# Kernel optimization log

Hardware: AMD Instinct MI355X
Metric: run time of the kernel (lower is better)

The kernel has to match this reference:

```python
import jax, jax.numpy as jnp
import numpy as np

D_MODEL = 1024
N_HEADS = 16
HEAD_DIM = D_MODEL // N_HEADS
MAX_LEN = 2048
BATCH = 2
SEQ = 2048


def setup_inputs() -> dict:
    key = jax.random.key(0)
    ks = jax.random.split(key, 6)
    std = 1.0 / np.sqrt(D_MODEL)
    x = jax.random.normal(ks[0], (BATCH, SEQ, D_MODEL), dtype=jnp.float32)
    Wqkv = jax.random.uniform(ks[1], (D_MODEL, 3 * D_MODEL), minval=-std, maxval=std, dtype=jnp.float32)
    bqkv = jax.random.uniform(ks[2], (3 * D_MODEL,), minval=-std, maxval=std, dtype=jnp.float32)
    Wout = jax.random.uniform(ks[3], (D_MODEL, D_MODEL), minval=-std, maxval=std, dtype=jnp.float32)
    bout = jax.random.uniform(ks[4], (D_MODEL,), minval=-std, maxval=std, dtype=jnp.float32)
    rel_pos_bias = 0.02 * jax.random.normal(ks[5], (2 * MAX_LEN - 1,), dtype=jnp.float32)
    return {"x": x, "Wqkv": Wqkv, "bqkv": bqkv, "Wout": Wout, "bout": bout, "rel_pos_bias": rel_pos_bias}


def reference(x, Wqkv, bqkv, Wout, bout, rel_pos_bias):
    B, S, _ = x.shape
    scale = HEAD_DIM ** -0.5
    qkv = x @ Wqkv + bqkv                       # [B,S,3*dm]
    qkv = qkv.reshape(B, S, 3, N_HEADS, HEAD_DIM)
    qkv = jnp.transpose(qkv, (2, 0, 3, 1, 4))   # [3,B,H,S,D]
    q, k, v = qkv[0], qkv[1], qkv[2]
    scores = jnp.einsum('bhqd,bhkd->bhqk', q, k) * scale
    pos = jnp.arange(S)
    rel = jnp.clip(pos[:, None] - pos[None, :] + (MAX_LEN - 1), 0, 2 * MAX_LEN - 2)
    scores = scores + rel_pos_bias[rel][None, None]  # bias shared over batch & heads
    probs = jax.nn.softmax(scores, axis=-1)
    out = jnp.einsum('bhqk,bhkd->bhqd', probs, v)    # [B,H,S,D]
    out = jnp.transpose(out, (0, 2, 1, 3)).reshape(B, S, D_MODEL)
    return out @ Wout + bout
```

## Files before the change

kernel.cpp:

```cpp
#include <hip/hip_runtime.h>
#include <cmath>

#define B_ 2
#define S_ 2048
#define H_ 16
#define D_ 64
#define DM 1024

typedef unsigned short u16;
using short8 = __attribute__((ext_vector_type(8))) short;
using f32x4  = __attribute__((ext_vector_type(4))) float;
using f32x16 = __attribute__((ext_vector_type(16))) float;
using i32x4  = __attribute__((ext_vector_type(4))) int;
typedef float uf4 __attribute__((ext_vector_type(4), aligned(4)));

__device__ __forceinline__ u16 f32_to_bf16(float f) {
    unsigned int u = __float_as_uint(f);
    u += 0x7fffu + ((u >> 16) & 1u);
    return (u16)(u >> 16);
}

__device__ __forceinline__ float exp2_fast(float x) {
    float r;
    asm("v_exp_f32 %0, %1" : "=v"(r) : "v"(x));
    return r;
}

__device__ __forceinline__ int cvt_pk_bf16(float lo, float hi) {
    int r;
    asm("v_cvt_pk_bf16_f32 %0, %1, %2" : "=v"(r) : "v"(lo), "v"(hi));
    return r;
}

__device__ __forceinline__ void gl_lds16(const void* src, void* dst) {
    __builtin_amdgcn_global_load_lds(
        (const __attribute__((address_space(1))) unsigned int*)src,
        (__attribute__((address_space(3))) unsigned int*)dst, 16, 0, 0);
}

__device__ __forceinline__ f32x16 mfma32(short8 a, short8 b, f32x16 c) {
    return __builtin_amdgcn_mfma_f32_32x32x16_bf16(a, b, c, 0, 0, 0);
}

__global__ __launch_bounds__(256) void relattn_prep(
    const float* __restrict__ x, const float* __restrict__ Wqkv,
    const float* __restrict__ Wout, const float* __restrict__ relb,
    u16* __restrict__ xb, u16* __restrict__ WqkvT, u16* __restrict__ WoutT,
    float* __restrict__ relb2)
{
    __shared__ float T[64][65];
    const int tid = threadIdx.x;
    int blk = blockIdx.x;
    if (blk >= 3072) {
        int i0 = ((blk - 3072) * 256 + tid) * 4;
#pragma unroll
        for (int j = 0; j < 4; ++j)
            if (i0 + j < 2 * 2048 - 1)
                relb2[i0 + j] = relb[i0 + j] * 1.44269504f;
        return;
    }
    if (blk < 2048) {
        size_t base = ((size_t)blk * 256 + tid) * 8;
        float4 v0 = *(const float4*)(x + base);
        float4 v1 = *(const float4*)(x + base + 4);
        ushort4 p0 = make_ushort4(f32_to_bf16(v0.x), f32_to_bf16(v0.y),
                                  f32_to_bf16(v0.z), f32_to_bf16(v0.w));
        ushort4 p1 = make_ushort4(f32_to_bf16(v1.x), f32_to_bf16(v1.y),
                                  f32_to_bf16(v1.z), f32_to_bf16(v1.w));
        *(ushort4*)(xb + base) = p0;
        *(ushort4*)(xb + base + 4) = p1;
        return;
    }
    int id = blk - 2048;
    const float* in; u16* outp; int R, C;
    if (id < 768) { in = Wqkv; outp = WqkvT; R = 1024; C = 3072; }
    else          { id -= 768; in = Wout;  outp = WoutT; R = 1024; C = 1024; }
    const int tpr = C >> 6;
    const int r0 = (id / tpr) << 6, c0 = (id % tpr) << 6;
#pragma unroll
    for (int it = 0; it < 4; ++it) {
        int e = tid + it * 256;
        int row = e >> 4, c4 = (e & 15) << 2;
        float4 v = *(const float4*)(in + (size_t)(r0 + row) * C + c0 + c4);
        T[row][c4 + 0] = v.x; T[row][c4 + 1] = v.y;
        T[row][c4 + 2] = v.z; T[row][c4 + 3] = v.w;
    }
    __syncthreads();
#pragma unroll
    for (int it = 0; it < 4; ++it) {
        int e = tid + it * 256;
        int crow = e >> 4, r4 = (e & 15) << 2;
        ushort4 pk = make_ushort4(f32_to_bf16(T[r4 + 0][crow]), f32_to_bf16(T[r4 + 1][crow]),
                                  f32_to_bf16(T[r4 + 2][crow]), f32_to_bf16(T[r4 + 3][crow]));
        *(ushort4*)(outp + (size_t)(c0 + crow) * R + r0 + r4) = pk;
    }
}

__global__ __launch_bounds__(256) void relattn_gemm_qkv(
    const u16* __restrict__ A, const u16* __restrict__ Bm,
    const float* __restrict__ bias, u16* __restrict__ qk, u16* __restrict__ Vt)
{
    __shared__ alignas(16) unsigned char AsB[16384];
    __shared__ alignas(16) unsigned char BsB[16384];
    const int tid = threadIdx.x;
    const int w = tid >> 6, l = tid & 63, ln = l & 15, hi = l >> 4;
    const int wr = w >> 1, wc = w & 1;
    const int row0 = blockIdx.y * 128, col0 = blockIdx.x * 128;
    const char* Ab = (const char*)A;
    const char* Bb = (const char*)Bm;

    f32x4 acc[4][4] = {};
    for (int step = 0; step < 16; ++step) {
        __syncthreads();
#pragma unroll
        for (int it = 0; it < 4; ++it) {
            int dsto = it * 4096 + w * 1024;
            int o = dsto + l * 16;
            int row = o >> 7;
            int swz = (o & 127) ^ ((row & 7) << 4);
            gl_lds16(Ab + (size_t)(row0 + row) * 2048 + step * 128 + swz, AsB + dsto);
            gl_lds16(Bb + (size_t)(col0 + row) * 2048 + step * 128 + swz, BsB + dsto);
        }
        __syncthreads();
#pragma unroll
        for (int kk = 0; kk < 2; ++kk) {
            short8 a[4], b[4];
            const int kb = hi * 16 + kk * 64;
#pragma unroll
            for (int m = 0; m < 4; ++m) {
                int row = wr * 64 + m * 16 + ln;
                a[m] = *(const short8*)(AsB + row * 128 + (kb ^ ((row & 7) << 4)));
            }
#pragma unroll
            for (int n = 0; n < 4; ++n) {
                int row = wc * 64 + n * 16 + ln;
                b[n] = *(const short8*)(BsB + row * 128 + (kb ^ ((row & 7) << 4)));
            }
#pragma unroll
            for (int m = 0; m < 4; ++m)
#pragma unroll
                for (int n = 0; n < 4; ++n)
                    acc[m][n] = __builtin_amdgcn_mfma_f32_16x16x32_bf16(a[m], b[n], acc[m][n], 0, 0, 0);
        }
    }

    const int t = col0 >> 10;
    const int bb = row0 >> 11;
    if (t < 2) {
#pragma unroll
        for (int n = 0; n < 4; ++n) {
            int c = col0 + wc * 64 + n * 16 + ln;
            int h = (c >> 6) & 15, d = c & 63;
            float bv = bias[c];
            u16* plane = qk + (size_t)((t * B_ + bb) * H_ + h) * S_ * D_;
#pragma unroll
            for (int m = 0; m < 4; ++m)
#pragma unroll
                for (int r = 0; r < 4; ++r) {
                    int s = (row0 + wr * 64 + m * 16 + hi * 4 + r) & (S_ - 1);
                    plane[(size_t)s * D_ + d] = f32_to_bf16(acc[m][n][r] + bv);
                }
        }
    } else {
#pragma unroll
        for (int n = 0; n < 4; ++n) {
            int c = col0 + wc * 64 + n * 16 + ln;
            int h = (c >> 6) & 15, d = c & 63;
            float bv = bias[c];
            u16* vrow = Vt + (size_t)((bb * H_ + h) * D_ + d) * S_;
#pragma unroll
            for (int m = 0; m < 4; ++m) {
                int s = (row0 + wr * 64 + m * 16 + hi * 4) & (S_ - 1);
                ushort4 pk = make_ushort4(f32_to_bf16(acc[m][n][0] + bv),
                                          f32_to_bf16(acc[m][n][1] + bv),
                                          f32_to_bf16(acc[m][n][2] + bv),
                                          f32_to_bf16(acc[m][n][3] + bv));
                *(ushort4*)(vrow + s) = pk;
            }
        }
    }
}

__global__ __launch_bounds__(512, 4) void relattn_attn(
    const u16* __restrict__ qk, const u16* __restrict__ Vt,
    const float* __restrict__ relb2, u16* __restrict__ aout)
{
    __shared__ alignas(16) unsigned char Lds[65536];
    const int tid = threadIdx.x;
    const int w = tid >> 6, l = tid & 63;
    const int wg = w & 3, g = w >> 2;
    const int l31 = l & 31, h2 = l >> 5;
    const int qt = blockIdx.x, bh = blockIdx.y;
    const int bb = bh >> 4;
    const char* qpl = (const char*)(qk + (size_t)bh * (S_ * D_));
    const char* kpl = (const char*)(qk + (size_t)(B_ * H_ + bh) * (S_ * D_));
    const char* vpl = (const char*)(Vt + (size_t)bh * (D_ * S_));
    unsigned char* GB = Lds + g * 32768;

    const int q0 = qt * 128 + wg * 32;
    const int qrow = q0 + l31;
    const int kvbase = g * 1024;

    short8 qf[4];
#pragma unroll
    for (int kd = 0; kd < 4; ++kd)
        qf[kd] = *(const short8*)(qpl + (size_t)qrow * 128 + kd * 32 + h2 * 16);

    f32x16 O0 = {}, O1 = {};
    float mrun = -1e30f, lrun = 0.f;

    {
#pragma unroll
        for (int it = 0; it < 2; ++it) {
            int dsto = it * 4096 + wg * 1024;
            int o = dsto + l * 16;
            int row = o >> 7;
            int swz = (o & 127) ^ ((row & 7) << 4);
            gl_lds16(kpl + (size_t)(kvbase + row) * 128 + swz, GB + dsto);
            gl_lds16(vpl + (size_t)row * (S_ * 2) + kvbase * 2 + swz, GB + 8192 + dsto);
        }
    }
    __syncthreads();

    for (int kt = 0; kt < 16; ++kt) {
        const int buf = kt & 1;
        const unsigned char* KB = GB + buf * 16384;
        const unsigned char* VB = KB + 8192;
        const int kv0 = kvbase + kt * 64;

        if (kt < 15) {
#pragma unroll
            for (int it = 0; it < 2; ++it) {
                int dsto = it * 4096 + wg * 1024;
                int o = dsto + l * 16;
                int row = o >> 7;
                int swz = (o & 127) ^ ((row & 7) << 4);
                unsigned char* db = GB + (buf ^ 1) * 16384 + dsto;
                gl_lds16(kpl + (size_t)(kv0 + 64 + row) * 128 + swz, db);
                gl_lds16(vpl + (size_t)row * (S_ * 2) + (kv0 + 64) * 2 + swz, db + 8192);
            }
        }

        const float* bp0 = relb2 + (qrow - kv0 - 4 * h2 + 2047);
        uf4 bv0[4], bv1[4];
#pragma unroll
        for (int rq = 0; rq < 4; ++rq) {
            bv0[rq] = *(const uf4*)(bp0 - 8 * rq - 3);
            bv1[rq] = *(const uf4*)(bp0 - 32 - 8 * rq - 3);
        }

        f32x16 s0 = {}, s1 = {};
        __builtin_amdgcn_s_setprio(1);
#pragma unroll
        for (int kd = 0; kd < 4; ++kd) {
            int kbyte = kd * 32 + h2 * 16;
            int sw = (l31 & 7) << 4;
            short8 k0 = *(const short8*)(KB + l31 * 128 + (kbyte ^ sw));
            short8 k1 = *(const short8*)(KB + (32 + l31) * 128 + (kbyte ^ sw));
            s0 = mfma32(k0, qf[kd], s0);
            s1 = mfma32(k1, qf[kd], s1);
        }
        __builtin_amdgcn_s_setprio(0);

        const float SC2 = 0.125f * 1.44269504f;
#pragma unroll
        for (int rq = 0; rq < 4; ++rq)
#pragma unroll
            for (int j = 0; j < 4; ++j) {
                s0[rq * 4 + j] = s0[rq * 4 + j] * SC2 + bv0[rq][3 - j];
                s1[rq * 4 + j] = s1[rq * 4 + j] * SC2 + bv1[rq][3 - j];
            }

        float a0 = fmaxf(fmaxf(s0[0], s0[1]), fmaxf(s0[2], s0[3]));
        float a1 = fmaxf(fmaxf(s0[4], s0[5]), fmaxf(s0[6], s0[7]));
        float a2 = fmaxf(fmaxf(s0[8], s0[9]), fmaxf(s0[10], s0[11]));
        float a3 = fmaxf(fmaxf(s0[12], s0[13]), fmaxf(s0[14], s0[15]));
        float a4 = fmaxf(fmaxf(s1[0], s1[1]), fmaxf(s1[2], s1[3]));
        float a5 = fmaxf(fmaxf(s1[4], s1[5]), fmaxf(s1[6], s1[7]));
        float a6 = fmaxf(fmaxf(s1[8], s1[9]), fmaxf(s1[10], s1[11]));
        float a7 = fmaxf(fmaxf(s1[12], s1[13]), fmaxf(s1[14], s1[15]));
        float tm = fmaxf(fmaxf(fmaxf(a0, a1), fmaxf(a2, a3)),
                         fmaxf(fmaxf(a4, a5), fmaxf(a6, a7)));
        tm = fmaxf(tm, __shfl_xor(tm, 32));

        if (!__all(tm - mrun <= 8.0f)) {
            float nm = fmaxf(mrun, tm);
            float al = exp2_fast(mrun - nm);
            mrun = nm;
            lrun *= al;
#pragma unroll
            for (int r = 0; r < 16; ++r) { O0[r] *= al; O1[r] *= al; }
        }

#pragma unroll
        for (int r = 0; r < 16; ++r) s0[r] = exp2_fast(s0[r] - mrun);
#pragma unroll
        for (int r = 0; r < 16; ++r) s1[r] = exp2_fast(s1[r] - mrun);
        float q0s = ((s0[0] + s0[1]) + (s0[2] + s0[3])) + ((s0[4] + s0[5]) + (s0[6] + s0[7]));
        float q1s = ((s0[8] + s0[9]) + (s0[10] + s0[11])) + ((s0[12] + s0[13]) + (s0[14] + s0[15]));
        float q2s = ((s1[0] + s1[1]) + (s1[2] + s1[3])) + ((s1[4] + s1[5]) + (s1[6] + s1[7]));
        float q3s = ((s1[8] + s1[9]) + (s1[10] + s1[11])) + ((s1[12] + s1[13]) + (s1[14] + s1[15]));
        float ps = (q0s + q1s) + (q2s + q3s);
        ps += __shfl_xor(ps, 32);
        lrun += ps;

        __builtin_amdgcn_s_setprio(1);
#pragma unroll
        for (int ts = 0; ts < 4; ++ts) {
            float p0, p1, p2, p3, p4, p5, p6, p7;
            if (ts == 0)      { p0=s0[0];  p1=s0[1];  p2=s0[2];  p3=s0[3];  p4=s0[4];  p5=s0[5];  p6=s0[6];  p7=s0[7]; }
            else if (ts == 1) { p0=s0[8];  p1=s0[9];  p2=s0[10]; p3=s0[11]; p4=s0[12]; p5=s0[13]; p6=s0[14]; p7=s0[15]; }
            else if (ts == 2) { p0=s1[0];  p1=s1[1];  p2=s1[2];  p3=s1[3];  p4=s1[4];  p5=s1[5];  p6=s1[6];  p7=s1[7]; }
            else              { p0=s1[8];  p1=s1[9];  p2=s1[10]; p3=s1[11]; p4=s1[12]; p5=s1[13]; p6=s1[14]; p7=s1[15]; }
            int c01 = cvt_pk_bf16(p0, p1), c23 = cvt_pk_bf16(p2, p3);
            int c45 = cvt_pk_bf16(p4, p5), c67 = cvt_pk_bf16(p6, p7);
            int px01 = __shfl_xor(c01, 32), px23 = __shfl_xor(c23, 32);
            int px45 = __shfl_xor(c45, 32), px67 = __shfl_xor(c67, 32);
            i32x4 pw;
            pw[0] = h2 ? px45 : c01;
            pw[1] = h2 ? px67 : c23;
            pw[2] = h2 ? c45 : px01;
            pw[3] = h2 ? c67 : px23;
            short8 pb = __builtin_bit_cast(short8, pw);
            int vbyte = ts * 32 + h2 * 16;
            int sw = (l31 & 7) << 4;
            short8 v0 = *(const short8*)(VB + l31 * 128 + (vbyte ^ sw));
            short8 v1 = *(const short8*)(VB + (32 + l31) * 128 + (vbyte ^ sw));
            O0 = mfma32(v0, pb, O0);
            O1 = mfma32(v1, pb, O1);
        }
        __builtin_amdgcn_s_setprio(0);
        __syncthreads();
    }

    {
        float* PO = (float*)(Lds + wg * 8704);
        float* PM = (float*)(Lds + wg * 8704 + 8192);
        float* PL = (float*)(Lds + wg * 8704 + 8448);
        if (g == 1) {
#pragma unroll
            for (int r = 0; r < 16; ++r) {
                PO[l * 32 + r] = O0[r];
                PO[l * 32 + 16 + r] = O1[r];
            }
            PM[l] = mrun;
            PL[l] = lrun;
        }
        __syncthreads();
        if (g == 1) return;
        float m1v = PM[l], l1v = PL[l];
        float nm = fmaxf(mrun, m1v);
        float a0m = exp2_fast(mrun - nm), a1m = exp2_fast(m1v - nm);
        float lr = lrun * a0m + l1v * a1m;
        float inv = 1.0f / lr;
        float f0 = a0m * inv, f1 = a1m * inv;
        const float* src = PO + l * 32;
        u16* orow = aout + (size_t)(bb * S_ + qrow) * DM + (bh & 15) * 64 + 4 * h2;
#pragma unroll
        for (int gq = 0; gq < 4; ++gq) {
            float o00 = O0[4*gq+0] * f0 + src[4*gq+0] * f1;
            float o01 = O0[4*gq+1] * f0 + src[4*gq+1] * f1;
            float o02 = O0[4*gq+2] * f0 + src[4*gq+2] * f1;
            float o03 = O0[4*gq+3] * f0 + src[4*gq+3] * f1;
            float o10 = O1[4*gq+0] * f0 + src[16+4*gq+0] * f1;
            float o11 = O1[4*gq+1] * f0 + src[16+4*gq+1] * f1;
            float o12 = O1[4*gq+2] * f0 + src[16+4*gq+2] * f1;
            float o13 = O1[4*gq+3] * f0 + src[16+4*gq+3] * f1;
            ushort4 w0 = make_ushort4(f32_to_bf16(o00), f32_to_bf16(o01), f32_to_bf16(o02), f32_to_bf16(o03));
            ushort4 w1 = make_ushort4(f32_to_bf16(o10), f32_to_bf16(o11), f32_to_bf16(o12), f32_to_bf16(o13));
            *(ushort4*)(orow + 8 * gq) = w0;
            *(ushort4*)(orow + 32 + 8 * gq) = w1;
        }
    }
}

__global__ __launch_bounds__(256) void relattn_gemm_out(
    const u16* __restrict__ A, const u16* __restrict__ Bm,
    const float* __restrict__ bias, float* __restrict__ out)
{
    __shared__ alignas(16) unsigned char AsB[16384];
    __shared__ alignas(16) unsigned char BsB[16384];
    const int tid = threadIdx.x;
    const int w = tid >> 6, l = tid & 63, ln = l & 15, hi = l >> 4;
    const int wr = w >> 1, wc = w & 1;
    const int row0 = blockIdx.y * 128, col0 = blockIdx.x * 128;
    const char* Ab = (const char*)A;
    const char* Bb = (const char*)Bm;

    f32x4 acc[4][4] = {};
    for (int step = 0; step < 16; ++step) {
        __syncthreads();
#pragma unroll
        for (int it = 0; it < 4; ++it) {
            int dsto = it * 4096 + w * 1024;
            int o = dsto + l * 16;
            int row = o >> 7;
            int swz = (o & 127) ^ ((row & 7) << 4);
            gl_lds16(Ab + (size_t)(row0 + row) * 2048 + step * 128 + swz, AsB + dsto);
            gl_lds16(Bb + (size_t)(col0 + row) * 2048 + step * 128 + swz, BsB + dsto);
        }
        __syncthreads();
#pragma unroll
        for (int kk = 0; kk < 2; ++kk) {
            short8 a[4], b[4];
            const int kb = hi * 16 + kk * 64;
#pragma unroll
            for (int m = 0; m < 4; ++m) {
                int row = wr * 64 + m * 16 + ln;
                a[m] = *(const short8*)(AsB + row * 128 + (kb ^ ((row & 7) << 4)));
            }
#pragma unroll
            for (int n = 0; n < 4; ++n) {
                int row = wc * 64 + n * 16 + ln;
                b[n] = *(const short8*)(BsB + row * 128 + (kb ^ ((row & 7) << 4)));
            }
#pragma unroll
            for (int m = 0; m < 4; ++m)
#pragma unroll
                for (int n = 0; n < 4; ++n)
                    acc[m][n] = __builtin_amdgcn_mfma_f32_16x16x32_bf16(a[m], b[n], acc[m][n], 0, 0, 0);
        }
    }

#pragma unroll
    for (int n = 0; n < 4; ++n) {
        int c = col0 + wc * 64 + n * 16 + ln;
        float bv = bias[c];
#pragma unroll
        for (int m = 0; m < 4; ++m)
#pragma unroll
            for (int r = 0; r < 4; ++r) {
                int row = row0 + wr * 64 + m * 16 + hi * 4 + r;
                out[(size_t)row * DM + c] = acc[m][n][r] + bv;
            }
    }
}

extern "C" void kernel_launch(void* const* d_in, const int* in_sizes, int n_in,
                              void* d_out, int out_size, void* d_ws, size_t ws_size,
                              hipStream_t stream) {
    const float* x    = (const float*)d_in[0];
    const float* Wqkv = (const float*)d_in[1];
    const float* bqkv = (const float*)d_in[2];
    const float* Wout = (const float*)d_in[3];
    const float* bout = (const float*)d_in[4];
    const float* relb = (const float*)d_in[5];
    float* out = (float*)d_out;

    u16* ws    = (u16*)d_ws;
    u16* xb    = ws;
    u16* WqkvT = xb + 4194304;
    u16* WoutT = WqkvT + 3145728;
    u16* qkpl  = WoutT + 1048576;
    u16* Vt    = qkpl + 8388608;
    u16* aout  = Vt + 4194304;
    float* relb2 = (float*)(aout + 4194304);

    relattn_prep<<<3076, 256, 0, stream>>>(x, Wqkv, Wout, relb, xb, WqkvT, WoutT, relb2);
    relattn_gemm_qkv<<<dim3(24, 32), 256, 0, stream>>>(xb, WqkvT, bqkv, qkpl, Vt);
    relattn_attn<<<dim3(16, 32), 512, 0, stream>>>(qkpl, Vt, relb2, aout);
    relattn_gemm_out<<<dim3(8, 32), 256, 0, stream>>>(aout, WoutT, bout, out);
}
```

Before: 149.1 us.

## Defer PV MFMA by one tile to overlap with next QK and softmax

The attention loop is software-pipelined. The P·V MFMAs for tile kt-1 now run right after the Q·K MFMAs of tile kt, so matrix work overlaps the exp/max softmax math of the current tile. V gets a triple-buffered LDS ring, LDS grows to 80 KB, bf16 P fragments are carried across iterations in registers, and a tail P·V step is added after the loop. The s_setprio hints are removed; the cost is higher register and LDS pressure.

```diff
diff --git a/kernel.cpp b/kernel.cpp
--- a/kernel.cpp
+++ b/kernel.cpp
@@ -185,7 +185,7 @@
     const u16* __restrict__ qk, const u16* __restrict__ Vt,
     const float* __restrict__ relb2, u16* __restrict__ aout)
 {
-    __shared__ alignas(16) unsigned char Lds[65536];
+    __shared__ alignas(16) unsigned char Lds[81920];
     const int tid = threadIdx.x;
     const int w = tid >> 6, l = tid & 63;
     const int wg = w & 3, g = w >> 2;
@@ -195,7 +195,8 @@
     const char* qpl = (const char*)(qk + (size_t)bh * (S_ * D_));
     const char* kpl = (const char*)(qk + (size_t)(B_ * H_ + bh) * (S_ * D_));
     const char* vpl = (const char*)(Vt + (size_t)bh * (D_ * S_));
-    unsigned char* GB = Lds + g * 32768;
+    unsigned char* GK = Lds + g * 40960;
+    unsigned char* GV = GK + 16384;
 
     const int q0 = qt * 128 + wg * 32;
     const int qrow = q0 + l31;
@@ -208,6 +209,7 @@
 
     f32x16 O0 = {}, O1 = {};
     float mrun = -1e30f, lrun = 0.f;
+    short8 pb[4];
 
     {
 #pragma unroll
@@ -216,16 +218,14 @@
             int o = dsto + l * 16;
             int row = o >> 7;
             int swz = (o & 127) ^ ((row & 7) << 4);
-            gl_lds16(kpl + (size_t)(kvbase + row) * 128 + swz, GB + dsto);
-            gl_lds16(vpl + (size_t)row * (S_ * 2) + kvbase * 2 + swz, GB + 8192 + dsto);
+            gl_lds16(kpl + (size_t)(kvbase + row) * 128 + swz, GK + dsto);
+            gl_lds16(vpl + (size_t)row * (S_ * 2) + kvbase * 2 + swz, GV + dsto);
         }
     }
     __syncthreads();
 
     for (int kt = 0; kt < 16; ++kt) {
-        const int buf = kt & 1;
-        const unsigned char* KB = GB + buf * 16384;
-        const unsigned char* VB = KB + 8192;
+        const unsigned char* KB = GK + (kt & 1) * 8192;
         const int kv0 = kvbase + kt * 64;
 
         if (kt < 15) {
@@ -235,9 +235,10 @@
                 int o = dsto + l * 16;
                 int row = o >> 7;
                 int swz = (o & 127) ^ ((row & 7) << 4);
-                unsigned char* db = GB + (buf ^ 1) * 16384 + dsto;
-                gl_lds16(kpl + (size_t)(kv0 + 64 + row) * 128 + swz, db);
-                gl_lds16(vpl + (size_t)row * (S_ * 2) + (kv0 + 64) * 2 + swz, db + 8192);
+                gl_lds16(kpl + (size_t)(kv0 + 64 + row) * 128 + swz,
+                         GK + ((kt + 1) & 1) * 8192 + dsto);
+                gl_lds16(vpl + (size_t)row * (S_ * 2) + (kv0 + 64) * 2 + swz,
+                         GV + ((kt + 1) % 3) * 8192 + dsto);
             }
         }
 
@@ -250,7 +251,6 @@
         }
 
         f32x16 s0 = {}, s1 = {};
-        __builtin_amdgcn_s_setprio(1);
 #pragma unroll
         for (int kd = 0; kd < 4; ++kd) {
             int kbyte = kd * 32 + h2 * 16;
@@ -260,7 +260,19 @@
             s0 = mfma32(k0, qf[kd], s0);
             s1 = mfma32(k1, qf[kd], s1);
         }
-        __builtin_amdgcn_s_setprio(0);
+
+        if (kt > 0) {
+            const unsigned char* VBp = GV + ((kt - 1) % 3) * 8192;
+#pragma unroll
+            for (int ts = 0; ts < 4; ++ts) {
+                int vbyte = ts * 32 + h2 * 16;
+                int sw = (l31 & 7) << 4;
+                short8 v0 = *(const short8*)(VBp + l31 * 128 + (vbyte ^ sw));
+                short8 v1 = *(const short8*)(VBp + (32 + l31) * 128 + (vbyte ^ sw));
+                O0 = mfma32(v0, pb[ts], O0);
+                O1 = mfma32(v1, pb[ts], O1);
+            }
+        }
 
         const float SC2 = 0.125f * 1.44269504f;
 #pragma unroll
@@ -304,7 +316,6 @@
         ps += __shfl_xor(ps, 32);
         lrun += ps;
 
-        __builtin_amdgcn_s_setprio(1);
 #pragma unroll
         for (int ts = 0; ts < 4; ++ts) {
             float p0, p1, p2, p3, p4, p5, p6, p7;
@@ -321,17 +332,24 @@
             pw[1] = h2 ? px67 : c23;
             pw[2] = h2 ? c45 : px01;
             pw[3] = h2 ? c67 : px23;
-            short8 pb = __builtin_bit_cast(short8, pw);
+            pb[ts] = __builtin_bit_cast(short8, pw);
+        }
+        __syncthreads();
+    }
+
+    {
+        const unsigned char* VBp = GV;
+#pragma unroll
+        for (int ts = 0; ts < 4; ++ts) {
             int vbyte = ts * 32 + h2 * 16;
             int sw = (l31 & 7) << 4;
-            short8 v0 = *(const short8*)(VB + l31 * 128 + (vbyte ^ sw));
-            short8 v1 = *(const short8*)(VB + (32 + l31) * 128 + (vbyte ^ sw));
-            O0 = mfma32(v0, pb, O0);
-            O1 = mfma32(v1, pb, O1);
-        }
-        __builtin_amdgcn_s_setprio(0);
-        __syncthreads();
-    }
+            short8 v0 = *(const short8*)(VBp + l31 * 128 + (vbyte ^ sw));
+            short8 v1 = *(const short8*)(VBp + (32 + l31) * 128 + (vbyte ^ sw));
+            O0 = mfma32(v0, pb[ts], O0);
+            O1 = mfma32(v1, pb[ts], O1);
+        }
+    }
+    __syncthreads();
 
     {
         float* PO = (float*)(Lds + wg * 8704);
```

After: 146.4 us. Within noise of the previous version (-1.8%).
